# Performance work log

Measured on AMD Instinct MI355X. Metric: run time of the kernel, lower is better.

Reference implementation:

```python
import jax, jax.numpy as jnp
import numpy as np

EMBED_DIM = 1024
HEAD_DIM = 64
B, T = 4, 4096


def setup_inputs() -> dict:
    key = jax.random.key(0)
    kx, kq, kk, kv = jax.random.split(key, 4)
    x = jax.random.normal(kx, (B, T, EMBED_DIM), dtype=jnp.float32)
    # nn.Linear weights, stored transposed as (in, out) for x @ W
    s = 1.0 / np.sqrt(EMBED_DIM)
    Wq = jax.random.normal(kq, (EMBED_DIM, HEAD_DIM), dtype=jnp.float32) * s
    Wk = jax.random.normal(kk, (EMBED_DIM, HEAD_DIM), dtype=jnp.float32) * s
    Wv = jax.random.normal(kv, (EMBED_DIM, HEAD_DIM), dtype=jnp.float32) * s
    return {"x": x, "Wq": Wq, "Wk": Wk, "Wv": Wv}


def reference(x, Wq, Wk, Wv):
    Bc, Tc, C = x.shape
    Q = x @ Wq  # [B, T, H]
    K = x @ Wk
    V = x @ Wv
    # NOTE: original scales by embedding_dim C, not head_dim
    scores = jnp.einsum('bqh,bkh->bqk', Q, K) / jnp.sqrt(jnp.float32(C))
    causal = jnp.tril(jnp.ones((Tc, Tc), dtype=bool))
    scores = jnp.where(causal, scores, -jnp.inf)
    attn = jax.nn.softmax(scores, axis=-1)
    return jnp.einsum('bqk,bkh->bqh', attn, V)
```

## Files before the change

kernel.cpp:

```cpp
#include <hip/hip_runtime.h>
#include <hip/hip_bf16.h>
#include <math.h>

typedef __attribute__((ext_vector_type(8))) short bf16x8;
typedef __attribute__((ext_vector_type(4))) float f32x4;

#define MFMA16 __builtin_amdgcn_mfma_f32_16x16x32_bf16

static constexpr int TSEQ = 4096;
static constexpr int EMB = 1024;
static constexpr int HD = 64;

__device__ __forceinline__ unsigned short f2bf(float f) {
    unsigned u = __builtin_bit_cast(unsigned, f);
    u += 0x7fffu + ((u >> 16) & 1u);
    return (unsigned short)(u >> 16);
}

__device__ __forceinline__ void gll16(const void* g, void* l) {
    __builtin_amdgcn_global_load_lds(
        (const __attribute__((address_space(1))) void*)g,
        (__attribute__((address_space(3))) void*)l, 16, 0, 0);
}

__global__ void prep_w(const float* __restrict__ Wq, const float* __restrict__ Wk,
                       const float* __restrict__ Wv, unsigned short* __restrict__ Wp) {
    int id = blockIdx.x * 256 + threadIdx.x;
    int wsel = id >> 16;
    int t = id & 65535;
    int k = t >> 6, n0 = t & 63;
    const float* W = (wsel == 0) ? Wq : (wsel == 1) ? Wk : Wv;
    float v = W[t];
    if (wsel == 0) v *= 0.03125f;
    int n = wsel * 64 + n0;
    Wp[(k >> 5) * 6144 + (n >> 4) * 512 + ((k >> 3) & 3) * 128 + (n & 15) * 8 + (k & 7)] = f2bf(v);
}

__global__ __launch_bounds__(1024, 4) void proj_kernel(const float* __restrict__ X,
        const unsigned short* __restrict__ Wp, unsigned short* __restrict__ Qp,
        unsigned short* __restrict__ Kp, unsigned short* __restrict__ Vp) {
    __shared__ unsigned short wlds[2][12288];
    __shared__ unsigned short xlds[2][4096];

    const int tid = threadIdx.x;
    const int lane = tid & 63, wave = tid >> 6;
    const int col = lane & 15, quad = lane >> 4;
    const int mq = wave >> 2, nw = wave & 3;
    const int row0 = blockIdx.x * 64;

    f32x4 acc[3];
#pragma unroll
    for (int j = 0; j < 3; j++) acc[j] = (f32x4)(0.0f);

    const char* wsrc = (const char*)Wp + lane * 16;
    auto stageW = [&](int p, int b) {
#pragma unroll
        for (int u = 0; u < 2; u++) {
            const char* s = wsrc + (size_t)(2 * p + u) * 12288;
            char* d = (char*)&wlds[b][0] + u * 12288;
            gll16(s + wave * 1024,       d + wave * 1024);
            gll16(s + (4 + wave) * 1024, d + (4 + wave) * 1024);
            gll16(s + (8 + wave) * 1024, d + (8 + wave) * 1024);
        }
    };
    const int u2 = tid - 256;
    const int xrow = u2 >> 3, q8 = u2 & 7;
    const bool xstager = (wave >= 4) && (wave < 12);
    const float* xsrc = xstager ? (X + (size_t)(row0 + xrow) * EMB + q8 * 8) : X;
    const int xo = (q8 >> 2) * 4096 + (xrow >> 4) * 1024 + (q8 & 3) * 256 + (xrow & 15) * 16;

    auto wr8 = [&](int b, float4 f0, float4 f1) {
        union { unsigned short s[8]; bf16x8 v; } r;
        r.s[0] = f2bf(f0.x); r.s[1] = f2bf(f0.y); r.s[2] = f2bf(f0.z); r.s[3] = f2bf(f0.w);
        r.s[4] = f2bf(f1.x); r.s[5] = f2bf(f1.y); r.s[6] = f2bf(f1.z); r.s[7] = f2bf(f1.w);
        *(bf16x8*)((char*)&xlds[b][0] + xo) = r.v;
    };
    auto compute = [&](int b) {
        bf16x8 A[2], Wf[2][3];
        const char* xb = (const char*)&xlds[b][0];
        const char* wb = (const char*)&wlds[b][0];
#pragma unroll
        for (int u = 0; u < 2; u++) {
            A[u] = *(const bf16x8*)(xb + u * 4096 + mq * 1024 + lane * 16);
#pragma unroll
            for (int j = 0; j < 3; j++)
                Wf[u][j] = *(const bf16x8*)(wb + u * 12288 + (j * 4 + nw) * 1024 + lane * 16);
        }
#pragma unroll
        for (int u = 0; u < 2; u++)
#pragma unroll
            for (int j = 0; j < 3; j++)
                acc[j] = MFMA16(A[u], Wf[u][j], acc[j], 0, 0, 0);
    };

    float4 pa0, pa1, qa0, qa1;
    if (wave < 4) {
        stageW(0, 0);
    } else if (xstager) {
        float4 t0 = *(const float4*)(xsrc);
        float4 t1 = *(const float4*)(xsrc + 4);
        wr8(0, t0, t1);
        pa0 = *(const float4*)(xsrc + 64);
        pa1 = *(const float4*)(xsrc + 68);
    }
    __syncthreads();

    for (int kci = 0; kci < 8; kci++) {
        const int s0 = kci * 2;
        if (xstager) {
            if (s0 + 2 < 16) {
                qa0 = *(const float4*)(xsrc + (s0 + 2) * 64);
                qa1 = *(const float4*)(xsrc + (s0 + 2) * 64 + 4);
            }
            if (s0 + 1 < 16) wr8(1, pa0, pa1);
        } else if (wave < 4) {
            if (s0 + 1 < 16) stageW(s0 + 1, 1);
        }
        compute(0);
        __syncthreads();
        if (xstager) {
            if (s0 + 3 < 16) {
                pa0 = *(const float4*)(xsrc + (s0 + 3) * 64);
                pa1 = *(const float4*)(xsrc + (s0 + 3) * 64 + 4);
            }
            if (s0 + 2 < 16) wr8(0, qa0, qa1);
        } else if (wave < 4) {
            if (s0 + 2 < 16) stageW(s0 + 2, 0);
        }
        compute(1);
        __syncthreads();
    }

    const int t = blockIdx.x * 4 + mq;
#pragma unroll
    for (int r = 0; r < 4; r++)
        Qp[t * 1024 + (nw >> 1) * 512 + (quad * 4 + r) * 32 +
           ((nw & 1) * 2 + (col >> 3)) * 8 + (col & 7)] = f2bf(acc[0][r]);
#pragma unroll
    for (int r = 0; r < 4; r++)
        Kp[(t * 2 + (nw >> 1)) * 512 + (quad * 4 + r) * 32 +
           ((nw & 1) * 2 + (col >> 3)) * 8 + (col & 7)] = f2bf(acc[1][r]);
    {
        ushort4 pk;
        pk.x = f2bf(acc[2][0]); pk.y = f2bf(acc[2][1]);
        pk.z = f2bf(acc[2][2]); pk.w = f2bf(acc[2][3]);
        *(ushort4*)&Vp[(t >> 1) * 2048 + nw * 512 + col * 32 + (t & 1) * 16 + quad * 4] = pk;
    }
}

__global__ __launch_bounds__(512, 4) void attn_kernel(const unsigned short* __restrict__ Qp,
        const unsigned short* __restrict__ Kp, const unsigned short* __restrict__ Vp,
        float* __restrict__ Out) {
    __shared__ float cmb[4][2][64][20];
    __shared__ unsigned short plds[8][2][640];
    const int lane = threadIdx.x & 63, wave = threadIdx.x >> 6;
    const int col = lane & 15, quad = lane >> 4;
    const int batch = blockIdx.x & 3;
    const int ti = 127 - (blockIdx.x >> 2);
    const int q0 = ti * 32;
    const size_t bT = (size_t)batch * TSEQ;
    const int fragoff = col * 64 + quad * 16;

    const char* QpB = (const char*)Qp;
    const char* KpB = (const char*)Kp;
    const char* VpB = (const char*)Vp;
    const int gt = (int)((bT + q0) >> 4);
    const int c0 = (int)(bT >> 5);

    bf16x8 aq[2][2];
#pragma unroll
    for (int m = 0; m < 2; m++)
#pragma unroll
        for (int h = 0; h < 2; h++)
            aq[m][h] = *(const bf16x8*)(QpB + (size_t)((gt + m) * 2 + h) * 1024 + fragoff);

    f32x4 o[2][4];
    f32x4 lsum[2];
#pragma unroll
    for (int m = 0; m < 2; m++) {
        lsum[m] = (f32x4)(0.0f);
#pragma unroll
        for (int t = 0; t < 4; t++) o[m][t] = (f32x4)(0.0f);
    }

    for (int c = wave; c <= ti; c += 8) {
        const char* kb = KpB + (size_t)(c0 + c) * 4096;
        const char* vb = VpB + (size_t)(c0 + c) * 4096;
        bf16x8 bk[2][2], bv[4];
#pragma unroll
        for (int j = 0; j < 2; j++)
#pragma unroll
            for (int h = 0; h < 2; h++)
                bk[j][h] = *(const bf16x8*)(kb + j * 2048 + h * 1024 + fragoff);
#pragma unroll
        for (int t = 0; t < 4; t++)
            bv[t] = *(const bf16x8*)(vb + t * 1024 + fragoff);

        f32x4 s[2][2];
#pragma unroll
        for (int m = 0; m < 2; m++)
#pragma unroll
            for (int j = 0; j < 2; j++) {
                f32x4 a = MFMA16(aq[m][0], bk[j][0], (f32x4)(0.0f), 0, 0, 0);
                s[m][j] = MFMA16(aq[m][1], bk[j][1], a, 0, 0, 0);
            }
        const bool diag = (c == ti);
#pragma unroll
        for (int m = 0; m < 2; m++)
#pragma unroll
            for (int j = 0; j < 2; j++)
#pragma unroll
                for (int r = 0; r < 4; r++) {
                    float v = s[m][j][r];
                    if (diag && (j * 16 + col > m * 16 + quad * 4 + r)) v = -INFINITY;
                    const float p = __expf(v);
                    lsum[m][r] += p;
                    plds[wave][m][(quad * 4 + r) * 40 + j * 16 + col] =
                        (unsigned short)(__builtin_bit_cast(unsigned, p) >> 16);
                }
        bf16x8 pa[2];
#pragma unroll
        for (int m = 0; m < 2; m++)
            pa[m] = *(const bf16x8*)(&plds[wave][m][col * 40 + quad * 8]);
#pragma unroll
        for (int m = 0; m < 2; m++)
#pragma unroll
            for (int t = 0; t < 4; t++)
                o[m][t] = MFMA16(pa[m], bv[t], o[m][t], 0, 0, 0);
    }

    auto wr = [&](int s) {
#pragma unroll
        for (int m = 0; m < 2; m++) {
#pragma unroll
            for (int t = 0; t < 4; t++)
                *(f32x4*)&cmb[s][m][lane][t * 4] = o[m][t];
            *(f32x4*)&cmb[s][m][lane][16] = lsum[m];
        }
    };
    auto rd = [&](int s) {
#pragma unroll
        for (int m = 0; m < 2; m++) {
#pragma unroll
            for (int t = 0; t < 4; t++)
                o[m][t] += *(const f32x4*)&cmb[s][m][lane][t * 4];
            lsum[m] += *(const f32x4*)&cmb[s][m][lane][16];
        }
    };
    if (wave >= 4) wr(wave - 4);
    __syncthreads();
    if (wave < 4) rd(wave);
    __syncthreads();
    if (wave == 2 || wave == 3) wr(wave);
    __syncthreads();
    if (wave < 2) rd(wave + 2);
    __syncthreads();
    if (wave == 1) wr(1);
    __syncthreads();
    if (wave == 0) {
        rd(1);
#pragma unroll
        for (int off = 1; off < 16; off <<= 1)
#pragma unroll
            for (int m = 0; m < 2; m++)
#pragma unroll
                for (int r = 0; r < 4; r++)
                    lsum[m][r] += __shfl_xor(lsum[m][r], off, 64);
#pragma unroll
        for (int m = 0; m < 2; m++)
#pragma unroll
            for (int r = 0; r < 4; r++) {
                const float inv = 1.0f / lsum[m][r];
                const size_t orow = (bT + q0 + m * 16 + quad * 4 + r) * HD;
#pragma unroll
                for (int t = 0; t < 4; t++)
                    Out[orow + t * 16 + col] = o[m][t][r] * inv;
            }
    }
}

extern "C" void kernel_launch(void* const* d_in, const int* in_sizes, int n_in,
                              void* d_out, int out_size, void* d_ws, size_t ws_size,
                              hipStream_t stream) {
    const float* x  = (const float*)d_in[0];
    const float* Wq = (const float*)d_in[1];
    const float* Wk = (const float*)d_in[2];
    const float* Wv = (const float*)d_in[3];
    float* out = (float*)d_out;

    char* w = (char*)d_ws;
    unsigned short* Wp = (unsigned short*)(w);
    unsigned short* Qp = (unsigned short*)(w + (512 << 10));
    unsigned short* Kp = (unsigned short*)(w + (512 << 10) + (2 << 20));
    unsigned short* Vp = (unsigned short*)(w + (512 << 10) + (4 << 20));

    hipLaunchKernelGGL(prep_w, dim3(768), dim3(256), 0, stream, Wq, Wk, Wv, Wp);
    hipLaunchKernelGGL(proj_kernel, dim3(256), dim3(1024), 0, stream, x, Wp, Qp, Kp, Vp);
    hipLaunchKernelGGL(attn_kernel, dim3(512), dim3(512), 0, stream, Qp, Kp, Vp, out);
}
```

Measured before the change: 140.4 us.

## Triple-buffer projection LDS stages with partial vmcnt waits and raw barriers

Moves the projection kernel from double to triple buffering of the W and X LDS tiles, so W staging via global_load_lds runs two steps ahead. __syncthreads is replaced with an explicit s_barrier plus hand-written s_waitcnt vmcnt(6)/lgkmcnt(0), which lets the next W stage stay in flight across the barrier. This is meant to hide global-load latency behind MFMA compute. In exchange it uses more LDS per block, which may limit occupancy, and it depends on the hand-tuned waitcnt counts being correct.

```diff
diff --git a/kernel.cpp b/kernel.cpp
--- a/kernel.cpp
+++ b/kernel.cpp
@@ -21,6 +21,15 @@
     __builtin_amdgcn_global_load_lds(
         (const __attribute__((address_space(1))) void*)g,
         (__attribute__((address_space(3))) void*)l, 16, 0, 0);
+}
+
+#define WAITV6 asm volatile("s_waitcnt vmcnt(6)" ::: "memory")
+#define WAITV0 asm volatile("s_waitcnt vmcnt(0)" ::: "memory")
+#define WAITLG asm volatile("s_waitcnt lgkmcnt(0)" ::: "memory")
+__device__ __forceinline__ void barrier_sync() {
+    asm volatile("" ::: "memory");
+    __builtin_amdgcn_s_barrier();
+    asm volatile("" ::: "memory");
 }
 
 __global__ void prep_w(const float* __restrict__ Wq, const float* __restrict__ Wk,
@@ -39,8 +48,8 @@
 __global__ __launch_bounds__(1024, 4) void proj_kernel(const float* __restrict__ X,
         const unsigned short* __restrict__ Wp, unsigned short* __restrict__ Qp,
         unsigned short* __restrict__ Kp, unsigned short* __restrict__ Vp) {
-    __shared__ unsigned short wlds[2][12288];
-    __shared__ unsigned short xlds[2][4096];
+    __shared__ unsigned short wlds[3][12288];
+    __shared__ unsigned short xlds[3][4096];
 
     const int tid = threadIdx.x;
     const int lane = tid & 63, wave = tid >> 6;
@@ -54,13 +63,14 @@
 
     const char* wsrc = (const char*)Wp + lane * 16;
     auto stageW = [&](int p, int b) {
+        char* d = (char*)wlds + b * 24576;
 #pragma unroll
         for (int u = 0; u < 2; u++) {
             const char* s = wsrc + (size_t)(2 * p + u) * 12288;
-            char* d = (char*)&wlds[b][0] + u * 12288;
-            gll16(s + wave * 1024,       d + wave * 1024);
-            gll16(s + (4 + wave) * 1024, d + (4 + wave) * 1024);
-            gll16(s + (8 + wave) * 1024, d + (8 + wave) * 1024);
+            char* du = d + u * 12288;
+            gll16(s + wave * 1024,       du + wave * 1024);
+            gll16(s + (4 + wave) * 1024, du + (4 + wave) * 1024);
+            gll16(s + (8 + wave) * 1024, du + (8 + wave) * 1024);
         }
     };
     const int u2 = tid - 256;
@@ -73,12 +83,12 @@
         union { unsigned short s[8]; bf16x8 v; } r;
         r.s[0] = f2bf(f0.x); r.s[1] = f2bf(f0.y); r.s[2] = f2bf(f0.z); r.s[3] = f2bf(f0.w);
         r.s[4] = f2bf(f1.x); r.s[5] = f2bf(f1.y); r.s[6] = f2bf(f1.z); r.s[7] = f2bf(f1.w);
-        *(bf16x8*)((char*)&xlds[b][0] + xo) = r.v;
+        *(bf16x8*)((char*)xlds + b * 8192 + xo) = r.v;
     };
     auto compute = [&](int b) {
         bf16x8 A[2], Wf[2][3];
-        const char* xb = (const char*)&xlds[b][0];
-        const char* wb = (const char*)&wlds[b][0];
+        const char* xb = (const char*)xlds + b * 8192;
+        const char* wb = (const char*)wlds + b * 24576;
 #pragma unroll
         for (int u = 0; u < 2; u++) {
             A[u] = *(const bf16x8*)(xb + u * 4096 + mq * 1024 + lane * 16);
@@ -93,42 +103,46 @@
                 acc[j] = MFMA16(A[u], Wf[u][j], acc[j], 0, 0, 0);
     };
 
+    int bc = 0, bx = 1, bw = 2;
     float4 pa0, pa1, qa0, qa1;
+
     if (wave < 4) {
         stageW(0, 0);
+        stageW(1, 1);
+        WAITV6;
     } else if (xstager) {
         float4 t0 = *(const float4*)(xsrc);
         float4 t1 = *(const float4*)(xsrc + 4);
         wr8(0, t0, t1);
         pa0 = *(const float4*)(xsrc + 64);
         pa1 = *(const float4*)(xsrc + 68);
-    }
-    __syncthreads();
-
-    for (int kci = 0; kci < 8; kci++) {
-        const int s0 = kci * 2;
-        if (xstager) {
-            if (s0 + 2 < 16) {
-                qa0 = *(const float4*)(xsrc + (s0 + 2) * 64);
-                qa1 = *(const float4*)(xsrc + (s0 + 2) * 64 + 4);
+        WAITLG;
+    }
+    barrier_sync();
+
+    auto step = [&](int s, float4& w0, float4& w1, float4& l0, float4& l1) {
+        if (wave < 4) {
+            if (s + 2 < 16) stageW(s + 2, bw);
+        } else if (xstager) {
+            if (s + 2 < 16) {
+                l0 = *(const float4*)(xsrc + (s + 2) * 64);
+                l1 = *(const float4*)(xsrc + (s + 2) * 64 + 4);
             }
-            if (s0 + 1 < 16) wr8(1, pa0, pa1);
-        } else if (wave < 4) {
-            if (s0 + 1 < 16) stageW(s0 + 1, 1);
-        }
-        compute(0);
-        __syncthreads();
-        if (xstager) {
-            if (s0 + 3 < 16) {
-                pa0 = *(const float4*)(xsrc + (s0 + 3) * 64);
-                pa1 = *(const float4*)(xsrc + (s0 + 3) * 64 + 4);
-            }
-            if (s0 + 2 < 16) wr8(0, qa0, qa1);
-        } else if (wave < 4) {
-            if (s0 + 2 < 16) stageW(s0 + 2, 0);
-        }
-        compute(1);
-        __syncthreads();
+            if (s + 1 < 16) wr8(bx, w0, w1);
+        }
+        compute(bc);
+        if (wave < 4) {
+            if (s + 2 < 16) { WAITV6; } else { WAITV0; }
+        } else if (xstager) {
+            WAITLG;
+        }
+        barrier_sync();
+        int t = bc; bc = bx; bx = bw; bw = t;
+    };
+
+    for (int si = 0; si < 8; si++) {
+        step(2 * si,     pa0, pa1, qa0, qa1);
+        step(2 * si + 1, qa0, qa1, pa0, pa1);
     }
 
     const int t = blockIdx.x * 4 + mq;
```

New measurement: 137.8 us. No clear change (-1.8%).
